# Kernel optimization log

Measured on AMD Instinct MI355X. Metric: run time of the kernel, lower is better.

Reference implementation:

```python
import jax, jax.numpy as jnp
import numpy as np

NUM_ANCHORS = 3
NUM_CLASSES = 80


def setup_inputs() -> dict:
    key = jax.random.key(0)
    k1, _ = jax.random.split(key)
    B, C, G0, G1 = 16, NUM_ANCHORS * (NUM_CLASSES + 5), 64, 64
    x = jax.random.normal(k1, (B, C, G0, G1), dtype=jnp.float32)
    # normalized (w, h) anchor pairs, as in __init__
    anchors = jnp.array([[0.28, 0.22], [0.38, 0.48], [0.90, 0.78]], dtype=jnp.float32)
    return {"x": x, "anchors": anchors}


def reference(x, anchors):
    B = x.shape[0]
    A, nC = NUM_ANCHORS, NUM_CLASSES
    g0, g1 = x.shape[2], x.shape[3]
    # [B, A, g0, g1, 5+nC]
    pred = x.reshape(B, A, nC + 5, g0, g1).transpose(0, 1, 3, 4, 2)

    sx = jax.nn.sigmoid(pred[..., 0])
    sy = jax.nn.sigmoid(pred[..., 1])
    w = pred[..., 2]
    h = pred[..., 3]
    pred_conf = jax.nn.sigmoid(pred[..., 4])
    pred_cls = jax.nn.sigmoid(pred[..., 5:])

    # grid_x varies along axis 2 (row index), grid_y along axis 3 (col index),
    # matching the torch repeat/.t() construction in compute_grid_offsets.
    grid_x = jnp.arange(g0, dtype=x.dtype).reshape(1, 1, g0, 1)
    grid_y = jnp.arange(g1, dtype=x.dtype).reshape(1, 1, 1, g1)
    anchor_w = (anchors[:, 0] * g0).reshape(1, A, 1, 1)
    anchor_h = (anchors[:, 1] * g1).reshape(1, A, 1, 1)

    pred_boxes = jnp.stack(
        [
            sx + grid_x,
            sy + grid_y,
            jnp.exp(w) * anchor_w,
            jnp.exp(h) * anchor_h,
        ],
        axis=-1,
    )  # [B, A, g0, g1, 4]

    scale = jnp.array([g0, g1, g0, g1], dtype=x.dtype)
    return pred_boxes / scale, pred_conf, pred_cls
```

## Files before the change

kernel.cpp:

```cpp
#include <hip/hip_runtime.h>
#include <math.h>

#define NB 16
#define NA 3
#define NC 80
#define GS 4096
#define NPOS (NB * NA * GS)
#define POSB 128
#define LSTR 133

__device__ __forceinline__ float sigmoidf_(float v) {
    return 1.0f / (1.0f + __expf(-v));
}

__global__ __launch_bounds__(256) void yolo_kernel(const float* __restrict__ x,
                                                   const float* __restrict__ anchors,
                                                   float* __restrict__ out) {
    __shared__ float lds[NC * LSTR];
    const int tid   = threadIdx.x;
    const int ba    = blockIdx.x >> 5;
    const int chunk = blockIdx.x & 31;
    const int s0    = chunk << 7;
    const float* __restrict__ xb = x + (size_t)ba * 85 * GS + s0;

    float tx = 0.f, ty = 0.f, tw = 0.f, th = 0.f, tc = 0.f;
    const bool box_lane = (tid < POSB);
    if (box_lane) {
        tx = xb[0 * GS + tid];
        ty = xb[1 * GS + tid];
        tw = xb[2 * GS + tid];
        th = xb[3 * GS + tid];
        tc = xb[4 * GS + tid];
    }

    const int p4  = tid & 31;
    const int chq = tid >> 5;
    const float* __restrict__ xc = xb + (size_t)(5 + chq) * GS + p4 * 4;
    float4 v[10];
    #pragma unroll
    for (int k = 0; k < 10; ++k)
        v[k] = *reinterpret_cast<const float4*>(xc + (size_t)(8 * k) * GS);

    if (box_lane) {
        const int p = s0 + tid;
        const int t = ba * GS + p;
        const int a = ba % NA;
        float4 box;
        box.x = (sigmoidf_(tx) + (float)(p >> 6)) * (1.0f / 64.0f);
        box.y = (sigmoidf_(ty) + (float)(p & 63)) * (1.0f / 64.0f);
        box.z = __expf(tw) * anchors[a * 2 + 0];
        box.w = __expf(th) * anchors[a * 2 + 1];
        reinterpret_cast<float4*>(out)[t] = box;
        out[(size_t)NPOS * 4 + t] = sigmoidf_(tc);
    }

    #pragma unroll
    for (int k = 0; k < 10; ++k) {
        const int ch = chq + 8 * k;
        float* lr = &lds[ch * LSTR + p4 * 4];
        lr[0] = sigmoidf_(v[k].x);
        lr[1] = sigmoidf_(v[k].y);
        lr[2] = sigmoidf_(v[k].z);
        lr[3] = sigmoidf_(v[k].w);
    }

    __syncthreads();

    float4* __restrict__ out4 =
        reinterpret_cast<float4*>(out + (size_t)NPOS * 5) + (size_t)(ba * GS + s0) * 20;
    #pragma unroll
    for (int k = 0; k < 10; ++k) {
        const int o4 = tid + (k << 8);
        const int p  = o4 / 20;
        const int c4 = o4 - p * 20;
        float4 w4;
        w4.x = lds[(c4 * 4 + 0) * LSTR + p];
        w4.y = lds[(c4 * 4 + 1) * LSTR + p];
        w4.z = lds[(c4 * 4 + 2) * LSTR + p];
        w4.w = lds[(c4 * 4 + 3) * LSTR + p];
        out4[o4] = w4;
    }
}

extern "C" void kernel_launch(void* const* d_in, const int* in_sizes, int n_in,
                              void* d_out, int out_size, void* d_ws, size_t ws_size,
                              hipStream_t stream) {
    const float* x       = (const float*)d_in[0];
    const float* anchors = (const float*)d_in[1];
    float* out           = (float*)d_out;
    const int blocks = NB * NA * 32;
    yolo_kernel<<<blocks, 256, 0, stream>>>(x, anchors, out);
}
```

Measured before the change: 112.6 us.

## Enlarge tiles to 256 positions and use XOR-swizzled float4 LDS transpose

Doubles the per-block position tile to 256 with 512 threads, so each block moves twice the data and there are half as many blocks. The padded-stride LDS layout is replaced by an XOR-swizzled layout, which allows float4 LDS writes while avoiding bank conflicts on the transposed reads. Class-channel loads are issued before the box loads. LDS use per block grows to 80KB, which may limit how many blocks fit per CU.

```diff
diff --git a/kernel.cpp b/kernel.cpp
--- a/kernel.cpp
+++ b/kernel.cpp
@@ -3,25 +3,31 @@
 
 #define NB 16
 #define NA 3
-#define NC 80
 #define GS 4096
 #define NPOS (NB * NA * GS)
-#define POSB 128
-#define LSTR 133
+#define POSB 256
 
 __device__ __forceinline__ float sigmoidf_(float v) {
     return 1.0f / (1.0f + __expf(-v));
 }
 
-__global__ __launch_bounds__(256) void yolo_kernel(const float* __restrict__ x,
-                                                   const float* __restrict__ anchors,
-                                                   float* __restrict__ out) {
-    __shared__ float lds[NC * LSTR];
+__global__ __launch_bounds__(512, 4) void yolo_kernel(const float* __restrict__ x,
+                                                      const float* __restrict__ anchors,
+                                                      float* __restrict__ out) {
+    __shared__ float lds[80 * POSB];
     const int tid   = threadIdx.x;
-    const int ba    = blockIdx.x >> 5;
-    const int chunk = blockIdx.x & 31;
-    const int s0    = chunk << 7;
+    const int w     = tid >> 6;
+    const int l     = tid & 63;
+    const int ba    = blockIdx.x >> 4;
+    const int chunk = blockIdx.x & 15;
+    const int s0    = chunk << 8;
     const float* __restrict__ xb = x + (size_t)ba * 85 * GS + s0;
+
+    const float* __restrict__ xc = xb + (size_t)(5 + w) * GS + l * 4;
+    float4 v[10];
+    #pragma unroll
+    for (int k = 0; k < 10; ++k)
+        v[k] = *reinterpret_cast<const float4*>(xc + (size_t)(8 * k) * GS);
 
     float tx = 0.f, ty = 0.f, tw = 0.f, th = 0.f, tc = 0.f;
     const bool box_lane = (tid < POSB);
@@ -33,13 +39,17 @@
         tc = xb[4 * GS + tid];
     }
 
-    const int p4  = tid & 31;
-    const int chq = tid >> 5;
-    const float* __restrict__ xc = xb + (size_t)(5 + chq) * GS + p4 * 4;
-    float4 v[10];
     #pragma unroll
-    for (int k = 0; k < 10; ++k)
-        v[k] = *reinterpret_cast<const float4*>(xc + (size_t)(8 * k) * GS);
+    for (int k = 0; k < 10; ++k) {
+        const int ch = w + 8 * k;
+        const int qs = l ^ ((ch >> 2) & 7);
+        float4 sv;
+        sv.x = sigmoidf_(v[k].x);
+        sv.y = sigmoidf_(v[k].y);
+        sv.z = sigmoidf_(v[k].z);
+        sv.w = sigmoidf_(v[k].w);
+        *reinterpret_cast<float4*>(&lds[ch * POSB + qs * 4]) = sv;
+    }
 
     if (box_lane) {
         const int p = s0 + tid;
@@ -54,30 +64,22 @@
         out[(size_t)NPOS * 4 + t] = sigmoidf_(tc);
     }
 
-    #pragma unroll
-    for (int k = 0; k < 10; ++k) {
-        const int ch = chq + 8 * k;
-        float* lr = &lds[ch * LSTR + p4 * 4];
-        lr[0] = sigmoidf_(v[k].x);
-        lr[1] = sigmoidf_(v[k].y);
-        lr[2] = sigmoidf_(v[k].z);
-        lr[3] = sigmoidf_(v[k].w);
-    }
-
     __syncthreads();
 
     float4* __restrict__ out4 =
         reinterpret_cast<float4*>(out + (size_t)NPOS * 5) + (size_t)(ba * GS + s0) * 20;
     #pragma unroll
     for (int k = 0; k < 10; ++k) {
-        const int o4 = tid + (k << 8);
+        const int o4 = tid + (k << 9);
         const int p  = o4 / 20;
         const int c4 = o4 - p * 20;
+        const int qs = (p >> 2) ^ (c4 & 7);
+        const int pb = p & 3;
         float4 w4;
-        w4.x = lds[(c4 * 4 + 0) * LSTR + p];
-        w4.y = lds[(c4 * 4 + 1) * LSTR + p];
-        w4.z = lds[(c4 * 4 + 2) * LSTR + p];
-        w4.w = lds[(c4 * 4 + 3) * LSTR + p];
+        w4.x = lds[(4 * c4 + 0) * POSB + qs * 4 + pb];
+        w4.y = lds[(4 * c4 + 1) * POSB + qs * 4 + pb];
+        w4.z = lds[(4 * c4 + 2) * POSB + qs * 4 + pb];
+        w4.w = lds[(4 * c4 + 3) * POSB + qs * 4 + pb];
         out4[o4] = w4;
     }
 }
@@ -88,6 +90,6 @@
     const float* x       = (const float*)d_in[0];
     const float* anchors = (const float*)d_in[1];
     float* out           = (float*)d_out;
-    const int blocks = NB * NA * 32;
-    yolo_kernel<<<blocks, 256, 0, stream>>>(x, anchors, out);
+    const int blocks = NB * NA * 16;
+    yolo_kernel<<<blocks, 512, 0, stream>>>(x, anchors, out);
 }
```

Result: no change. 112.2 us (-0.3%).
